# Kernel optimization log

Hardware: AMD Instinct MI355X
Metric: run time of the kernel (lower is better)

The kernel has to match this reference:

```python
import jax, jax.numpy as jnp
import numpy as np

B = 262144
HIST = 24
FORE = 20
HID = 256
# torch: tau_int = clamp(tau,1,18).long().item(); default tau=6.0 -> static 6 (host sync in torch)
TAU_INT = 6


def setup_inputs() -> dict:
    key = jax.random.key(0)
    ks = jax.random.split(key, 9)
    s = 0.1
    return {
        "history": jax.random.normal(ks[0], (B, HIST), jnp.float32),
        "enc_w1": jax.random.normal(ks[1], (HIST + FORE, HID), jnp.float32) * s,
        "enc_b1": jnp.zeros((HID,), jnp.float32),
        "enc_w2": jax.random.normal(ks[2], (HID, HID), jnp.float32) * s,
        "enc_b2": jnp.zeros((HID,), jnp.float32),
        "cor_w1": jax.random.normal(ks[3], (HID, HID), jnp.float32) * s,
        "cor_b1": jnp.zeros((HID,), jnp.float32),
        "cor_w2": jax.random.normal(ks[4], (HID, FORE), jnp.float32) * s,
        "cor_b2": jnp.zeros((FORE,), jnp.float32),
        "alpha": jnp.float32(0.2),
        "beta": jnp.float32(0.3),
        "gamma": jnp.float32(0.01),
        "tau": jnp.float32(6.0),
        "lambda_mix": jnp.float32(0.5),
    }


def _physics_core(history, alpha, beta, gamma, steps):
    a = jax.nn.sigmoid(alpha)
    b = jax.nn.sigmoid(beta)
    g = jnp.abs(gamma)
    T0 = history[:, -1]                      # [B]
    buf0 = history[:, -TAU_INT:].T           # [tau, B]; buf0[0] = history[:, -tau]

    def step(carry, _):
        T, buf = carry
        T_delayed = buf[0]
        T_new = T - a * T - b * T_delayed - g * T ** 3
        buf = jnp.concatenate([buf[1:], T_new[None, :]], axis=0)
        return (T_new, buf), T_new

    _, preds = jax.lax.scan(step, (T0, buf0), None, length=steps)
    return preds.T                            # [B, steps]


def reference(history, enc_w1, enc_b1, enc_w2, enc_b2,
              cor_w1, cor_b1, cor_w2, cor_b2,
              alpha, beta, gamma, tau, lambda_mix):
    T_physics = _physics_core(history, alpha, beta, gamma, FORE)   # [B, FORE]
    combined = jnp.concatenate([history, T_physics], axis=1)       # [B, HIST+FORE]
    h = jnp.tanh(combined @ enc_w1 + enc_b1)
    features = jnp.tanh(h @ enc_w2 + enc_b2)
    c = jnp.tanh(features @ cor_w1 + cor_b1)
    T_soft = c @ cor_w2 + cor_b2                                   # [B, FORE]
    lam = jax.nn.sigmoid(lambda_mix)
    T_pred = T_physics + lam * T_soft
    return (T_pred, T_physics, T_soft)
```

## Files before the change

kernel.cpp:

```cpp
#include <hip/hip_runtime.h>
#include <hip/hip_bf16.h>

#define NROWS 262144
#define HISTC 24
#define FOREC 20

typedef __bf16        v8bf __attribute__((ext_vector_type(8)));
typedef float         v4f  __attribute__((ext_vector_type(4)));
typedef float         v2f  __attribute__((ext_vector_type(2)));
typedef unsigned int  v4u  __attribute__((ext_vector_type(4)));
typedef unsigned int  v2u  __attribute__((ext_vector_type(2)));

#define WS_WT1_OFF 64
#define WT1_ELEMS 16384
#define WT2_ELEMS 65536
#define WT3_ELEMS 65536
#define WT4R_ELEMS 65536

#define TANH_C 2.885390081777927f

__device__ __forceinline__ unsigned short f2bf(float x) {
    unsigned u = __builtin_bit_cast(unsigned, x);
    u += 0x7FFFu + ((u >> 16) & 1u);
    return (unsigned short)(u >> 16);
}

__device__ __forceinline__ unsigned packbf2(float a, float b) {
    unsigned ua = __builtin_bit_cast(unsigned, a) + 0x8000u;
    unsigned ub = __builtin_bit_cast(unsigned, b) + 0x8000u;
    return __builtin_amdgcn_perm(ub, ua, 0x07060302u);
}

__device__ __forceinline__ void lds_barrier() {
    asm volatile("s_waitcnt lgkmcnt(0)\n\ts_barrier" ::: "memory");
}

__device__ __forceinline__ int swzi(int r, int byteoff) {
    return (r << 8) + (((byteoff) ^ ((r & 7) << 4)) >> 1);
}

__global__ void prep_kernel(const float* __restrict__ w1, const float* __restrict__ w2,
                            const float* __restrict__ w3, const float* __restrict__ w4,
                            const float* __restrict__ alpha, const float* __restrict__ beta,
                            const float* __restrict__ gamma, const float* __restrict__ lmix,
                            unsigned char* __restrict__ ws)
{
    if (blockIdx.x == 104) {
        int t = threadIdx.x;
        float* wsf = (float*)ws;
        if (t == 0) wsf[0] = 1.0f / (1.0f + expf(-alpha[0]));
        else if (t == 1) wsf[1] = 1.0f / (1.0f + expf(-beta[0]));
        else if (t == 2) wsf[2] = fabsf(gamma[0]);
        else if (t == 3) wsf[3] = 1.0f / (1.0f + expf(-lmix[0]));
        return;
    }
    int idx = (blockIdx.x * 256 + threadIdx.x) * 8;
    const float* src;
    int KT, Kreal, Nreal, srcN, local, ntmask;
    unsigned short* dst = (unsigned short*)(ws + WS_WT1_OFF);
    if (idx < WT1_ELEMS) {
        local = idx; src = w1; KT = 2; Kreal = 44; Nreal = 256; srcN = 256; ntmask = 255;
    } else if (idx < WT1_ELEMS + WT2_ELEMS) {
        local = idx - WT1_ELEMS; dst += WT1_ELEMS;
        src = w2; KT = 8; Kreal = 256; Nreal = 256; srcN = 256; ntmask = 255;
    } else if (idx < WT1_ELEMS + WT2_ELEMS + WT3_ELEMS) {
        local = idx - (WT1_ELEMS + WT2_ELEMS); dst += WT1_ELEMS + WT2_ELEMS;
        src = w3; KT = 8; Kreal = 256; Nreal = 256; srcN = 256; ntmask = 255;
    } else {
        local = idx - (WT1_ELEMS + WT2_ELEMS + WT3_ELEMS);
        dst += WT1_ELEMS + WT2_ELEMS + WT3_ELEMS;
        src = w4; KT = 8; Kreal = 256; Nreal = 20; srcN = 20; ntmask = 1;
    }
    int L   = (local >> 3) & 63;
    int blk = local >> 9;
    int kt = blk % KT, nt = (blk / KT) & ntmask;
    int cc = L & 15,  qq = L >> 4;
    int feat = nt * 16 + cc;
    int kbase = kt * 32 + qq * 8;
    unsigned short tmp[8];
#pragma unroll
    for (int j = 0; j < 8; ++j) {
        int k = kbase + j;
        float v = (k < Kreal && feat < Nreal) ? src[k * srcN + feat] : 0.0f;
        tmp[j] = f2bf(v);
    }
    v4u pk;
    pk[0] = tmp[0] | ((unsigned)tmp[1] << 16);
    pk[1] = tmp[2] | ((unsigned)tmp[3] << 16);
    pk[2] = tmp[4] | ((unsigned)tmp[5] << 16);
    pk[3] = tmp[6] | ((unsigned)tmp[7] << 16);
    *(v4u*)&dst[local] = pk;
}

template<int KT, int KTN>
__device__ __forceinline__ void layer_pipe(unsigned short* buf,
        const v4u* __restrict__ wp, const v4u* __restrict__ wpn,
        const float* __restrict__ bias, v4u A[2][2],
        int w, int c, int q, int lane)
{
    v4f acc[2][4];
#pragma unroll
    for (int ft = 0; ft < 2; ++ft)
#pragma unroll
        for (int st = 0; st < 4; ++st) {
            v4f z = {0.0f, 0.0f, 0.0f, 0.0f};
            acc[ft][st] = z;
        }

#pragma unroll
    for (int kt = 0; kt < KT; ++kt) {
        const int cs = kt & 1;
        const int ps = cs ^ 1;
        if (kt + 1 < KT) {
#pragma unroll
            for (int ft = 0; ft < 2; ++ft)
                A[ps][ft] = wp[((w * 2 + ft) * KT + kt + 1) * 64 + lane];
        } else {
#pragma unroll
            for (int ft = 0; ft < 2; ++ft)
                A[ps][ft] = wpn[((w * 2 + ft) * KTN + 0) * 64 + lane];
        }
#pragma unroll
        for (int st = 0; st < 4; ++st) {
            v4u braw = *(const v4u*)&buf[swzi(st * 16 + c, kt * 64 + q * 16)];
            v8bf bb = __builtin_bit_cast(v8bf, braw);
#pragma unroll
            for (int ft = 0; ft < 2; ++ft)
                acc[ft][st] = __builtin_amdgcn_mfma_f32_16x16x32_bf16(
                    __builtin_bit_cast(v8bf, A[cs][ft]), bb, acc[ft][st], 0, 0, 0);
        }
    }

    lds_barrier();

#pragma unroll
    for (int ft = 0; ft < 2; ++ft) {
        v4f bi = *(const v4f*)&bias[w * 32 + ft * 16 + q * 4];
        v4f bic;
#pragma unroll
        for (int r = 0; r < 4; ++r) bic[r] = bi[r] * TANH_C;
#pragma unroll
        for (int st = 0; st < 4; ++st) {
            float x[4];
#pragma unroll
            for (int r = 0; r < 4; ++r) {
                float t = __builtin_fmaf(acc[ft][st][r], TANH_C, bic[r]);
                float p = __builtin_amdgcn_exp2f(t);
                float rc = __builtin_amdgcn_rcpf(p + 1.0f);
                x[r] = __builtin_fmaf(-2.0f, rc, 1.0f);
            }
            v2u d; d[0] = packbf2(x[0], x[1]); d[1] = packbf2(x[2], x[3]);
            *(v2u*)&buf[swzi(st * 16 + c, w * 64 + ft * 32 + q * 8)] = d;
        }
    }
    lds_barrier();
}

__global__ __launch_bounds__(512, 6) void fused_kernel(
    const float* __restrict__ history,
    const float* __restrict__ eb1, const float* __restrict__ eb2,
    const float* __restrict__ cb1, const float* __restrict__ cb2,
    const unsigned char* __restrict__ ws, float* __restrict__ out)
{
    __shared__ unsigned short buf[64 * 256];
    __shared__ float tp[64 * 20];

    const int tid  = threadIdx.x;
    const int w    = tid >> 6;
    const int lane = tid & 63;
    const int c    = lane & 15;
    const int q    = lane >> 4;
    const int row0 = blockIdx.x << 6;
    const float* wsf = (const float*)ws;
    const v4u* wp1 = (const v4u*)(ws + WS_WT1_OFF);
    const v4u* wp2 = wp1 + WT1_ELEMS / 8;
    const v4u* wp3 = wp2 + WT2_ELEMS / 8;
    const v4u* wp4 = wp3 + WT3_ELEMS / 8;

    v4u A[2][2];
#pragma unroll
    for (int ft = 0; ft < 2; ++ft)
        A[0][ft] = wp1[((w * 2 + ft) * 2 + 0) * 64 + lane];

    if (tid < 384) {
        int r  = tid / 6, c4 = tid - r * 6;
        v4f h4 = *(const v4f*)&history[(long)(row0 + r) * 24 + c4 * 4];
        v2u d; d[0] = packbf2(h4[0], h4[1]); d[1] = packbf2(h4[2], h4[3]);
        *(v2u*)&buf[swzi(r, c4 * 8)] = d;
    }
    if (tid < 320) {
        int r = tid / 5, g = tid - r * 5;
        v2u z = {0u, 0u};
        *(v2u*)&buf[swzi(r, 88 + g * 8)] = z;
    }
    if (tid < 64) {
        const float* hrow = &history[(long)(row0 + tid) * 24];
        v2f h18 = *(const v2f*)&hrow[18];
        v4f h20 = *(const v4f*)&hrow[20];
        float pa = wsf[0], pb = wsf[1], pg = wsf[2];
        float d0 = h18[0], d1 = h18[1], d2 = h20[0];
        float d3 = h20[1], d4 = h20[2], d5 = h20[3];
        float T = d5;
#pragma unroll
        for (int s = 0; s < 20; ++s) {
            float t3 = T * T * T;
            float Tn = T - pa * T;
            Tn = Tn - pb * d0;
            Tn = Tn - pg * t3;
            tp[tid * 20 + s] = Tn;
            buf[swzi(tid, 48 + 2 * s)] = f2bf(Tn);
            d0 = d1; d1 = d2; d2 = d3; d3 = d4; d4 = d5; d5 = Tn;
            T = Tn;
        }
    }
    lds_barrier();

    layer_pipe<2, 8>(buf, wp1, wp2, eb1, A, w, c, q, lane);
    layer_pipe<8, 8>(buf, wp2, wp3, eb2, A, w, c, q, lane);
    layer_pipe<8, 8>(buf, wp3, wp4, cb1, A, w, c, q, lane);

    const int sw = w >> 1, fw = w & 1;
    v4f acc4 = {0.0f, 0.0f, 0.0f, 0.0f};
    v4u wa = fw ? A[0][1] : A[0][0];
#pragma unroll
    for (int kt = 0; kt < 8; ++kt) {
        v4u wn;
        if (kt + 1 < 8)
            wn = wp4[((w * 2 + fw) * 8 + kt + 1) * 64 + lane];
        v4u braw = *(const v4u*)&buf[swzi(sw * 16 + c, kt * 64 + q * 16)];
        v8bf bb = __builtin_bit_cast(v8bf, braw);
        acc4 = __builtin_amdgcn_mfma_f32_16x16x32_bf16(
            __builtin_bit_cast(v8bf, wa), bb, acc4, 0, 0, 0);
        if (kt + 1 < 8) wa = wn;
    }

    const float lam = wsf[3];
    const long sample = (long)row0 + sw * 16 + c;
    float* outP = out;
    float* outF = out + (long)NROWS * 20;
    float* outS = out + (long)NROWS * 40;
    if (fw == 0) {
        int f0 = q * 4;
        v4f bi  = *(const v4f*)&cb2[f0];
        v4f tph = *(const v4f*)&tp[(sw * 16 + c) * 20 + f0];
        v4f ts, pr;
#pragma unroll
        for (int r = 0; r < 4; ++r) {
            ts[r] = acc4[r] + bi[r];
            pr[r] = tph[r] + lam * ts[r];
        }
        *(v4f*)&outS[sample * 20 + f0] = ts;
        *(v4f*)&outP[sample * 20 + f0] = pr;
        *(v4f*)&outF[sample * 20 + f0] = tph;
    } else if (q == 0) {
        v4f bi  = *(const v4f*)&cb2[16];
        v4f tph = *(const v4f*)&tp[(sw * 16 + c) * 20 + 16];
        v4f ts, pr;
#pragma unroll
        for (int r = 0; r < 4; ++r) {
            ts[r] = acc4[r] + bi[r];
            pr[r] = tph[r] + lam * ts[r];
        }
        *(v4f*)&outS[sample * 20 + 16] = ts;
        *(v4f*)&outP[sample * 20 + 16] = pr;
        *(v4f*)&outF[sample * 20 + 16] = tph;
    }
}

extern "C" void kernel_launch(void* const* d_in, const int* in_sizes, int n_in,
                              void* d_out, int out_size, void* d_ws, size_t ws_size,
                              hipStream_t stream)
{
    const float* history = (const float*)d_in[0];
    const float* enc_w1  = (const float*)d_in[1];
    const float* enc_b1  = (const float*)d_in[2];
    const float* enc_w2  = (const float*)d_in[3];
    const float* enc_b2  = (const float*)d_in[4];
    const float* cor_w1  = (const float*)d_in[5];
    const float* cor_b1  = (const float*)d_in[6];
    const float* cor_w2  = (const float*)d_in[7];
    const float* cor_b2  = (const float*)d_in[8];
    const float* alpha   = (const float*)d_in[9];
    const float* beta    = (const float*)d_in[10];
    const float* gamma   = (const float*)d_in[11];
    const float* lmix    = (const float*)d_in[13];

    prep_kernel<<<105, 256, 0, stream>>>(enc_w1, enc_w2, cor_w1, cor_w2,
                                         alpha, beta, gamma, lmix,
                                         (unsigned char*)d_ws);
    fused_kernel<<<NROWS / 64, 512, 0, stream>>>(history, enc_b1, enc_b2, cor_b1, cor_b2,
                                                 (const unsigned char*)d_ws, (float*)d_out);
}
```

Measured before the change: 199.7 us.

## Deepen weight prefetch to two stages and double-buffer LDS B-fragment loads

Weight fragments now go through a three-slot ring so each one is loaded from global memory two k-steps ahead, carrying across layer boundaries. Activation fragments from LDS are also double-buffered, loading the next k-step's B operands before the current MFMAs run. Swizzled LDS addresses are precomputed once per thread as byte offsets instead of calling swzi in every loop. The launch bound drops from 6 to 4 blocks per CU so the extra registers fit, at the cost of lower occupancy.

```diff
diff --git a/kernel.cpp b/kernel.cpp
--- a/kernel.cpp
+++ b/kernel.cpp
@@ -92,11 +92,12 @@
     *(v4u*)&dst[local] = pk;
 }
 
-template<int KT, int KTN>
-__device__ __forceinline__ void layer_pipe(unsigned short* buf,
+template<int KT, int KTN, int S0>
+__device__ __forceinline__ void layer_pipe(char* bufc,
         const v4u* __restrict__ wp, const v4u* __restrict__ wpn,
-        const float* __restrict__ bias, v4u A[2][2],
-        int w, int c, int q, int lane)
+        const float* __restrict__ bias, v4u A[3][2],
+        const int* be, const int* bo, const int* wAo, const int* wBo,
+        int w, int q, int lane)
 {
     v4f acc[2][4];
 #pragma unroll
@@ -107,23 +108,33 @@
             acc[ft][st] = z;
         }
 
+    v4u Bf[2][4];
+#pragma unroll
+    for (int st = 0; st < 4; ++st)
+        Bf[0][st] = *(const v4u*)(bufc + be[st]);
+
 #pragma unroll
     for (int kt = 0; kt < KT; ++kt) {
-        const int cs = kt & 1;
-        const int ps = cs ^ 1;
+        const int cs = (S0 + kt) % 3;
+        const int ps = (S0 + kt + 2) % 3;
+        if (kt + 2 < KT) {
+#pragma unroll
+            for (int ft = 0; ft < 2; ++ft)
+                A[ps][ft] = wp[((w * 2 + ft) * KT + kt + 2) * 64 + lane];
+        } else {
+#pragma unroll
+            for (int ft = 0; ft < 2; ++ft)
+                A[ps][ft] = wpn[((w * 2 + ft) * KTN + (kt + 2 - KT)) * 64 + lane];
+        }
         if (kt + 1 < KT) {
-#pragma unroll
-            for (int ft = 0; ft < 2; ++ft)
-                A[ps][ft] = wp[((w * 2 + ft) * KT + kt + 1) * 64 + lane];
-        } else {
-#pragma unroll
-            for (int ft = 0; ft < 2; ++ft)
-                A[ps][ft] = wpn[((w * 2 + ft) * KTN + 0) * 64 + lane];
+            const int kn = kt + 1;
+#pragma unroll
+            for (int st = 0; st < 4; ++st)
+                Bf[kn & 1][st] = *(const v4u*)(bufc + ((kn & 1) ? bo[st] : be[st]) + kn * 64);
         }
 #pragma unroll
         for (int st = 0; st < 4; ++st) {
-            v4u braw = *(const v4u*)&buf[swzi(st * 16 + c, kt * 64 + q * 16)];
-            v8bf bb = __builtin_bit_cast(v8bf, braw);
+            v8bf bb = __builtin_bit_cast(v8bf, Bf[kt & 1][st]);
 #pragma unroll
             for (int ft = 0; ft < 2; ++ft)
                 acc[ft][st] = __builtin_amdgcn_mfma_f32_16x16x32_bf16(
@@ -150,13 +161,13 @@
                 x[r] = __builtin_fmaf(-2.0f, rc, 1.0f);
             }
             v2u d; d[0] = packbf2(x[0], x[1]); d[1] = packbf2(x[2], x[3]);
-            *(v2u*)&buf[swzi(st * 16 + c, w * 64 + ft * 32 + q * 8)] = d;
+            *(v2u*)(bufc + (ft ? wBo[st] : wAo[st])) = d;
         }
     }
     lds_barrier();
 }
 
-__global__ __launch_bounds__(512, 6) void fused_kernel(
+__global__ __launch_bounds__(512, 4) void fused_kernel(
     const float* __restrict__ history,
     const float* __restrict__ eb1, const float* __restrict__ eb2,
     const float* __restrict__ cb1, const float* __restrict__ cb2,
@@ -164,6 +175,7 @@
 {
     __shared__ unsigned short buf[64 * 256];
     __shared__ float tp[64 * 20];
+    char* bufc = (char*)buf;
 
     const int tid  = threadIdx.x;
     const int w    = tid >> 6;
@@ -177,10 +189,30 @@
     const v4u* wp3 = wp2 + WT2_ELEMS / 8;
     const v4u* wp4 = wp3 + WT3_ELEMS / 8;
 
-    v4u A[2][2];
-#pragma unroll
-    for (int ft = 0; ft < 2; ++ft)
+    const int e    = (c >> 2) & 1;
+    const int d64  = e << 6;
+    const int qp_r = (q * 16) ^ ((c & 3) << 4);
+    const int qp_w = (q * 8) ^ ((c & 1) << 4);
+    const int x5b  = (c >> 1) & 1;
+    const int wsh  = (w ^ e) << 6;
+    const int fA   = x5b << 5;
+    int be[4], bo[4], wAo[4], wBo[4];
+#pragma unroll
+    for (int st = 0; st < 4; ++st) {
+        int b0 = (st * 16 + c) * 512 + qp_r;
+        be[st] = b0 + d64;
+        bo[st] = b0 - d64;
+        int wb = (st * 16 + c) * 512 + qp_w + wsh;
+        wAo[st] = wb + fA;
+        wBo[st] = wb + 32 - fA;
+    }
+
+    v4u A[3][2];
+#pragma unroll
+    for (int ft = 0; ft < 2; ++ft) {
         A[0][ft] = wp1[((w * 2 + ft) * 2 + 0) * 64 + lane];
+        A[1][ft] = wp1[((w * 2 + ft) * 2 + 1) * 64 + lane];
+    }
 
     if (tid < 384) {
         int r  = tid / 6, c4 = tid - r * 6;
@@ -215,23 +247,29 @@
     }
     lds_barrier();
 
-    layer_pipe<2, 8>(buf, wp1, wp2, eb1, A, w, c, q, lane);
-    layer_pipe<8, 8>(buf, wp2, wp3, eb2, A, w, c, q, lane);
-    layer_pipe<8, 8>(buf, wp3, wp4, cb1, A, w, c, q, lane);
+    layer_pipe<2, 8, 0>(bufc, wp1, wp2, eb1, A, be, bo, wAo, wBo, w, q, lane);
+    layer_pipe<8, 8, 2>(bufc, wp2, wp3, eb2, A, be, bo, wAo, wBo, w, q, lane);
+    layer_pipe<8, 8, 1>(bufc, wp3, wp4, cb1, A, be, bo, wAo, wBo, w, q, lane);
 
     const int sw = w >> 1, fw = w & 1;
+    const int b04 = (sw * 16 + c) * 512 + qp_r;
+    const int be4 = b04 + d64, bo4 = b04 - d64;
     v4f acc4 = {0.0f, 0.0f, 0.0f, 0.0f};
     v4u wa = fw ? A[0][1] : A[0][0];
+    v4u wb = fw ? A[1][1] : A[1][0];
+    v4u bcur = *(const v4u*)(bufc + be4);
 #pragma unroll
     for (int kt = 0; kt < 8; ++kt) {
         v4u wn;
+        if (kt + 2 < 8)
+            wn = wp4[((w * 2 + fw) * 8 + kt + 2) * 64 + lane];
+        v4u bnext;
         if (kt + 1 < 8)
-            wn = wp4[((w * 2 + fw) * 8 + kt + 1) * 64 + lane];
-        v4u braw = *(const v4u*)&buf[swzi(sw * 16 + c, kt * 64 + q * 16)];
-        v8bf bb = __builtin_bit_cast(v8bf, braw);
+            bnext = *(const v4u*)(bufc + (((kt + 1) & 1) ? bo4 : be4) + (kt + 1) * 64);
         acc4 = __builtin_amdgcn_mfma_f32_16x16x32_bf16(
-            __builtin_bit_cast(v8bf, wa), bb, acc4, 0, 0, 0);
-        if (kt + 1 < 8) wa = wn;
+            __builtin_bit_cast(v8bf, wa), __builtin_bit_cast(v8bf, bcur), acc4, 0, 0, 0);
+        if (kt + 1 < 8) { wa = wb; bcur = bnext; }
+        if (kt + 2 < 8) wb = wn;
     }
 
     const float lam = wsf[3];
```

Result: slower. 206.7 us (+3.5%).
